# Optimization experiments

Hardware: AMD Instinct MI355X
Metric: run time of the kernel (lower is better)

The kernel has to match this reference:

```python
import jax, jax.numpy as jnp
import numpy as np
from jax import lax

S_DET, S_ANG = 725, 360   # detector bins, projection angles
OUT = 512                 # reconstructed image side
NNZ = 8388608             # nonzeros in sparse backprojection matrix AT
BATCH = 4
BN_EPS = 1e-3             # keras BatchNormalization default epsilon


def _ramp_filter():
    # w_bfunction(pi, linspace(-362, 362, 725))
    s = np.linspace(-np.floor(S_DET / 2), S_DET - np.floor(S_DET / 2) - 1, S_DET)
    v = np.pi * s
    u = np.empty_like(v)
    z = v == 0
    u[z] = 0.5
    nz = ~z
    u[nz] = (np.cos(v[nz]) - 1.0) / v[nz] ** 2 + np.sin(v[nz]) / v[nz]
    return (u * np.pi ** 2 / (4.0 * np.pi ** 2)).astype(np.float32)


def setup_inputs() -> dict:
    key = jax.random.key(0)
    ks = jax.random.split(key, 24)
    p = 0.05
    inp = {
        'inputs': jax.random.normal(ks[0], (BATCH, S_DET, S_ANG, 1), jnp.float32),
        'w_sin1': jax.random.normal(ks[1], (5, 5, 1, 64), jnp.float32) * p,
        'b_sin1': jnp.zeros((64,), jnp.float32),
        'w_sin_mid': jax.random.normal(ks[2], (4, 5, 5, 64, 64), jnp.float32) * p,
        'sin_gamma': jnp.ones((4, 64), jnp.float32),
        'sin_beta': jnp.zeros((4, 64), jnp.float32),
        'sin_mean': jax.random.normal(ks[3], (4, 64), jnp.float32) * 0.1,
        'sin_var': jax.random.uniform(ks[4], (4, 64), jnp.float32, 0.5, 1.5),
        'w_sin6': jax.random.normal(ks[5], (5, 5, 64, 1), jnp.float32) * p,
        'b_sin6': jnp.zeros((1,), jnp.float32),
        'w_ct1': jax.random.normal(ks[6], (5, 5, 1, 64), jnp.float32) * p,
        'b_ct1': jnp.zeros((64,), jnp.float32),
        'w_ct_mid': jax.random.normal(ks[7], (5, 5, 5, 64, 64), jnp.float32) * p,
        'ct_gamma': jnp.ones((5, 64), jnp.float32),
        'ct_beta': jnp.zeros((5, 64), jnp.float32),
        'ct_mean': jax.random.normal(ks[8], (5, 64), jnp.float32) * 0.1,
        'ct_var': jax.random.uniform(ks[9], (5, 64), jnp.float32, 0.5, 1.5),
        'w_ct6': jax.random.normal(ks[10], (5, 5, 64, 1), jnp.float32) * p,
        'b_ct6': jnp.zeros((1,), jnp.float32),
        'w_b': jnp.asarray(_ramp_filter()),
        'at_vals': jax.random.uniform(ks[11], (NNZ,), jnp.float32) * 1e-3,
        'at_rows': jnp.sort(jax.random.randint(ks[12], (NNZ,), 0, OUT * OUT, jnp.int32)),
        'at_cols': jax.random.randint(ks[13], (NNZ,), 0, S_DET * S_ANG, jnp.int32),
    }
    return inp


def _conv2d(x, w, b=None):
    y = lax.conv_general_dilated(x, w, (1, 1), 'SAME',
                                 dimension_numbers=('NHWC', 'HWIO', 'NHWC'))
    return y if b is None else y + b


def _bn(x, g, b, m, v):
    return (x - m) * (g * lax.rsqrt(v + BN_EPS)) + b


def _decode(sin_fan, w_b, at_vals, at_rows, at_cols):
    B = sin_fan.shape[0]
    sf = jnp.transpose(sin_fan, (0, 2, 1, 3))          # [B, 360, 725, 1]
    x = sf.reshape(-1, S_DET, 1)                       # [B*360, 725, 1]
    k = w_b.reshape(S_DET, 1, 1)
    f = lax.conv_general_dilated(x, k, (1,), 'SAME',
                                 dimension_numbers=('NWC', 'WIO', 'NWC'))
    f2 = f.reshape(B, -1).T                            # [261000, B]
    # sparse AT @ f2 via gather + segment_sum
    contrib = at_vals[:, None] * f2[at_cols]           # [nnz, B]
    rf = jax.ops.segment_sum(contrib, at_rows, num_segments=OUT * OUT)
    return 4.0 * rf.T.reshape(B, OUT, OUT, 1)


def reference(inputs, w_sin1, b_sin1, w_sin_mid, sin_gamma, sin_beta, sin_mean,
              sin_var, w_sin6, b_sin6, w_ct1, b_ct1, w_ct_mid, ct_gamma,
              ct_beta, ct_mean, ct_var, w_ct6, b_ct6, w_b, at_vals,
              at_rows, at_cols):
    # --- sinogram domain residual CNN ---
    de = jax.nn.relu(_conv2d(inputs, w_sin1, b_sin1))
    pp = de
    for i in range(4):  # M1 residual blocks
        de = jax.nn.relu(_bn(_conv2d(de, w_sin_mid[i]), sin_gamma[i],
                             sin_beta[i], sin_mean[i], sin_var[i]))
        pp = de + pp
    de_sin = _conv2d(pp / 4.0, w_sin6, b_sin6) + inputs
    # --- filtered backprojection ---
    fbp = _decode(de_sin, w_b, at_vals, at_rows, at_cols)
    # --- image domain residual CNN ---
    out = jax.nn.relu(_conv2d(fbp, w_ct1, b_ct1))
    qq = out
    for i in range(5):  # M2 residual blocks
        out = jax.nn.relu(_bn(_conv2d(out, w_ct_mid[i]), ct_gamma[i],
                              ct_beta[i], ct_mean[i], ct_var[i]))
        qq = qq + out
    outputs = _conv2d(qq / 5.0, w_ct6, b_ct6) + fbp
    return (de_sin, outputs, fbp)
```

## Files before the change

### kernel.cpp

```cpp
#include <hip/hip_runtime.h>
#include <stdint.h>

#define S_DET 725
#define S_ANG 360
#define OUTD  512
#define NB    4

typedef float    float4v __attribute__((ext_vector_type(4)));
typedef int      int4v   __attribute__((ext_vector_type(4)));
typedef _Float16 half8   __attribute__((ext_vector_type(8)));
typedef _Float16 half4   __attribute__((ext_vector_type(4)));
typedef _Float16 half2v  __attribute__((ext_vector_type(2)));

#define GAS __attribute__((address_space(1)))
#define LAS __attribute__((address_space(3)))

__device__ __forceinline__ void async16(const void* src, void* lds) {
  __builtin_amdgcn_global_load_lds((const GAS void*)(uintptr_t)src,
                                   (LAS void*)(uint32_t)(uintptr_t)lds, 16, 0, 0);
}

__global__ __launch_bounds__(256)
void prep_weights(const float* __restrict__ wsin, const float* __restrict__ sg,
                  const float* __restrict__ sb,  const float* __restrict__ sm,
                  const float* __restrict__ sv,
                  const float* __restrict__ wct, const float* __restrict__ cg,
                  const float* __restrict__ cbt, const float* __restrict__ cm,
                  const float* __restrict__ cv,
                  const float* __restrict__ wsin6, const float* __restrict__ wct6,
                  _Float16* __restrict__ wout, float* __restrict__ bout,
                  _Float16* __restrict__ w6out)
{
  int id = blockIdx.x * 256 + threadIdx.x;
  if (id < 9 * 102400) {
    int l   = id / 102400;
    int rem = id - l * 102400;
    int t = rem >> 12;
    int kn = rem & 4095;
    int k = kn >> 6, n = kn & 63;
    const float *w, *g, *b, *m, *v;
    if (l < 4) { w = wsin + l*102400; g = sg + l*64; b = sb + l*64; m = sm + l*64; v = sv + l*64; }
    else { int li = l - 4; w = wct + li*102400; g = cg + li*64; b = cbt + li*64; m = cm + li*64; v = cv + li*64; }
    float s = g[n] * rsqrtf(v[n] + 1e-3f);
    float val = w[rem] * s;
    int slot = (k >> 3) ^ (n & 7);
    wout[(size_t)l*102400 + t*4096 + n*64 + slot*8 + (k & 7)] = (_Float16)val;
    if (rem < 64)
      bout[l*64 + rem] = b[rem] - m[rem] * s;
  } else {
    int r = id - 9 * 102400;
    if (r < 3200)
      w6out[r] = (_Float16)(r < 1600 ? wsin6[r] : wct6[r - 1600]);
  }
}

template <int IMG>
__global__ __launch_bounds__(256)
void conv1_kernel(const float* __restrict__ src, _Float16* __restrict__ dst,
                  const float* __restrict__ w1, const float* __restrict__ b1,
                  int H, int W, int b0)
{
  __shared__ __align__(16) float in_s[400];
  __shared__ __align__(16) float w_s[1600];
  __shared__ float b_s[64];
  const int tid = threadIdx.x;
  const int bz = blockIdx.z, gb = b0 + bz;
  const int y0 = blockIdx.y * 16, x0 = blockIdx.x * 16;
  for (int i = tid; i < 1600; i += 256) w_s[i] = w1[i];
  if (tid < 64) b_s[tid] = b1[tid];
  for (int i = tid; i < 400; i += 256) {
    int iy = i / 20, ix = i - iy * 20;
    int y = y0 - 2 + iy, x = x0 - 2 + ix;
    float v = 0.f;
    if (y >= 0 && y < H && x >= 0 && x < W) {
      if (IMG) v = 4.f * src[(size_t)(y * W + x) * 4 + gb];
      else     v = src[((size_t)gb * H + y) * W + x];
    }
    in_s[i] = v;
  }
  __syncthreads();
  const int ty = tid >> 4, tx = tid & 15;
  float acc[64];
#pragma unroll
  for (int c = 0; c < 64; ++c) acc[c] = 0.f;
  int dy = 0, dx = 0;
  for (int t = 0; t < 25; ++t) {
    float v = in_s[(ty + dy) * 20 + tx + dx];
    const float4v* wp = (const float4v*)(w_s + t * 64);
#pragma unroll
    for (int c = 0; c < 16; ++c) {
      float4v w4 = wp[c];
      acc[4*c+0] += v * w4[0]; acc[4*c+1] += v * w4[1];
      acc[4*c+2] += v * w4[2]; acc[4*c+3] += v * w4[3];
    }
    if (++dx == 5) { dx = 0; ++dy; }
  }
  const int y = y0 + ty, x = x0 + tx;
  if (y < H && x < W) {
    uint32_t* dp = (uint32_t*)(dst + ((size_t)(bz * H + y) * W + x) * 64);
#pragma unroll
    for (int c = 0; c < 32; ++c) {
      float v0 = acc[2*c]   + b_s[2*c];   v0 = v0 > 0.f ? v0 : 0.f;
      float v1 = acc[2*c+1] + b_s[2*c+1]; v1 = v1 > 0.f ? v1 : 0.f;
      half2v h = { (_Float16)v0, (_Float16)v1 };
      dp[c] = __builtin_bit_cast(uint32_t, h);
    }
  }
}

__global__ __launch_bounds__(256, 2)
void mid_conv(const _Float16* __restrict__ src, _Float16* __restrict__ dst,
              float* __restrict__ accum,
              const _Float16* __restrict__ wt, const _Float16* __restrict__ w6g,
              const float* __restrict__ bias, const char* __restrict__ zbuf,
              int H, int W, int b0)
{
  __shared__ __align__(16) char smem[51200 + 2 * 8192 + 3200 + 16];
  char* const atile = smem;
  char* const wbuf  = smem + 51200;
  _Float16* const w6l = (_Float16*)(smem + 51200 + 16384);
  char* const zl = smem + 51200 + 16384 + 3200;
  const int tid = threadIdx.x;
  const int wv = tid >> 6, ln = tid & 63;
  const int bz = blockIdx.z, gb = b0 + bz;
  const int y0 = blockIdx.y * 16, x0 = blockIdx.x * 16;

  if (tid < 200) ((half8*)w6l)[tid] = ((const half8*)w6g)[tid];
  if (tid < 4) ((int*)zl)[tid] = 0;

  for (int inst = wv; inst < 50; inst += 4) {
    const int slot = inst * 64 + ln;
    const int p = slot >> 3, gp = slot & 7;
    const int g = gp ^ (p & 7);
    const int iy = p / 20, ix = p - iy * 20;
    const int y = y0 - 2 + iy, x = x0 - 2 + ix;
    const char* sp = (y >= 0 && y < H && x >= 0 && x < W)
        ? (const char*)(src + ((size_t)(bz * H + y) * W + x) * 64) + g * 16
        : zbuf + g * 16;
    async16(sp, atile + inst * 1024);
  }
#pragma unroll
  for (int j = 0; j < 2; ++j) {
    const int inst = wv * 2 + j;
    async16((const char*)wt + inst * 1024 + ln * 16, wbuf + inst * 1024);
  }
  __syncthreads();

  float4v acc[4][4];
  float4v acc6[4];
#pragma unroll
  for (int pi = 0; pi < 4; ++pi) {
    acc6[pi] = (float4v){0.f, 0.f, 0.f, 0.f};
#pragma unroll
    for (int ci = 0; ci < 4; ++ci) acc[pi][ci] = (float4v){0.f, 0.f, 0.f, 0.f};
  }

  int dy = 0, dx = 0;
  for (int t = 0; t < 25; ++t) {
    if (t < 24) {
      char* wdst = wbuf + ((t + 1) & 1) * 8192;
#pragma unroll
      for (int j = 0; j < 2; ++j) {
        const int inst = wv * 2 + j;
        async16((const char*)wt + (t + 1) * 8192 + inst * 1024 + ln * 16,
                wdst + inst * 1024);
      }
    }
    const char* wb = wbuf + (t & 1) * 8192;
#pragma unroll
    for (int kc = 0; kc < 2; ++kc) {
      const int g0 = kc * 4 + (ln >> 4);
      half8 wf[4], af[4], wf6;
#pragma unroll
      for (int ci = 0; ci < 4; ++ci) {
        const int ch = ci * 16 + (ln & 15);
        wf[ci] = *(const half8*)(wb + ch * 128 + ((g0 ^ (ch & 7)) << 4));
      }
      wf6 = *(const half8*)((ln & 15) == 0
                ? (const char*)(w6l + t * 64 + kc * 32 + ((ln >> 4) << 3))
                : zl);
#pragma unroll
      for (int pi = 0; pi < 4; ++pi) {
        const int p = (wv * 4 + pi + dy) * 20 + (ln & 15) + dx;
        af[pi] = *(const half8*)(atile + p * 128 + ((g0 ^ (p & 7)) << 4));
      }
#pragma unroll
      for (int pi = 0; pi < 4; ++pi) {
#pragma unroll
        for (int ci = 0; ci < 4; ++ci)
          acc[pi][ci] = __builtin_amdgcn_mfma_f32_16x16x32_f16(
              wf[ci], af[pi], acc[pi][ci], 0, 0, 0);
        acc6[pi] = __builtin_amdgcn_mfma_f32_16x16x32_f16(
            wf6, af[pi], acc6[pi], 0, 0, 0);
      }
    }
    if (++dx == 5) { dx = 0; ++dy; }
    __syncthreads();
  }

  const int tx = ln & 15;
  const int x = x0 + tx;
#pragma unroll
  for (int pi = 0; pi < 4; ++pi) {
    const int y = y0 + wv * 4 + pi;
    if (y < H && x < W) {
      _Float16* dp = dst + ((size_t)(bz * H + y) * W + x) * 64;
#pragma unroll
      for (int ci = 0; ci < 4; ++ci) {
        const int cbase = ci * 16 + (ln >> 4) * 4;
        const float4v bv = *(const float4v*)(bias + cbase);
        half4 h;
#pragma unroll
        for (int r = 0; r < 4; ++r) {
          float v = acc[pi][ci][r] + bv[r];
          v = v > 0.f ? v : 0.f;
          h[r] = (_Float16)v;
        }
        *(half4*)(dp + cbase) = h;
      }
    }
  }
  if (ln < 16) {
#pragma unroll
    for (int pi = 0; pi < 4; ++pi) {
      const int y = y0 + wv * 4 + pi, x2 = x0 + ln;
      if (y < H && x2 < W)
        accum[((size_t)gb * H + y) * W + x2] += acc6[pi][0];
    }
  }
}

__global__ __launch_bounds__(256, 2)
void fc_accum(const _Float16* __restrict__ src, float* __restrict__ accum,
              const float* __restrict__ w6, const char* __restrict__ zbuf,
              int H, int W, int b0)
{
  __shared__ __align__(16) char smem[51200 + 3200];
  char* const atile = smem;
  _Float16* const wl = (_Float16*)(smem + 51200);
  const int tid = threadIdx.x;
  const int wv = tid >> 6, ln = tid & 63;
  const int bz = blockIdx.z, gb = b0 + bz;
  const int y0 = blockIdx.y * 16, x0 = blockIdx.x * 16;
  for (int i = tid; i < 1600; i += 256) wl[i] = (_Float16)w6[i];
  for (int inst = wv; inst < 50; inst += 4) {
    const int slot = inst * 64 + ln;
    const int p = slot >> 3, gp = slot & 7;
    const int g = gp ^ (p & 7);
    const int iy = p / 20, ix = p - iy * 20;
    const int y = y0 - 2 + iy, x = x0 - 2 + ix;
    const char* sp = (y >= 0 && y < H && x >= 0 && x < W)
        ? (const char*)(src + ((size_t)(bz * H + y) * W + x) * 64) + g * 16
        : zbuf + g * 16;
    async16(sp, atile + inst * 1024);
  }
  __syncthreads();
  const int ty = tid >> 4, tx = tid & 15;
  float sum = 0.f;
  int dy = 0, dxx = 0;
  for (int t = 0; t < 25; ++t) {
    const int p = (ty + dy) * 20 + tx + dxx;
    const char* pb = atile + p * 128;
    const int pk = p & 7;
    const half2v* wp = (const half2v*)(wl + t * 64);
#pragma unroll
    for (int g = 0; g < 8; ++g) {
      half8 h = *(const half8*)(pb + ((g ^ pk) << 4));
#pragma unroll
      for (int q = 0; q < 4; ++q) {
        half2v a = { h[2*q], h[2*q+1] };
        sum = __builtin_amdgcn_fdot2(a, wp[g * 4 + q], sum, false);
      }
    }
    if (++dxx == 5) { dxx = 0; ++dy; }
  }
  const int y = y0 + ty, x = x0 + tx;
  if (y < H && x < W) accum[((size_t)gb * H + y) * W + x] += sum;
}

__global__ __launch_bounds__(256)
void write_desin(const float* __restrict__ accf, const float* __restrict__ inputs,
                 const float* __restrict__ b6, float* __restrict__ out)
{
  int id = blockIdx.x * 256 + threadIdx.x;
  if (id < NB * S_DET * S_ANG) out[id] = accf[id] * 0.25f + b6[0] + inputs[id];
}

__global__ __launch_bounds__(128)
void ramp_filter(const float* __restrict__ desin, const float* __restrict__ wb,
                 _Float16* __restrict__ f2h)
{
  __shared__ float col[1472];
  __shared__ float wl[725];
  const int blk = blockIdx.x;
  const int b = blk / 360, a = blk - b * 360;
  const int tid = threadIdx.x;
  for (int i = tid; i < 1472; i += 128) col[i] = 0.f;
  for (int i = tid; i < 725; i += 128) wl[i] = wb[i];
  __syncthreads();
  for (int i = tid; i < 725; i += 128) col[368 + i] = desin[(b * 725 + i) * 360 + a];
  __syncthreads();
  const int s0 = tid * 6;
  if (s0 < 725) {
    float o0 = 0, o1 = 0, o2 = 0, o3 = 0, o4 = 0, o5 = 0;
    const float* cb = col + 6 + s0;
    float r0 = cb[0], r1 = cb[1], r2 = cb[2], r3 = cb[3], r4 = cb[4], r5 = cb[5];
    for (int t = 0; t < 725; ++t) {
      float w = wl[t];
      o0 += r0 * w; o1 += r1 * w; o2 += r2 * w;
      o3 += r3 * w; o4 += r4 * w; o5 += r5 * w;
      r0 = r1; r1 = r2; r2 = r3; r3 = r4; r4 = r5; r5 = cb[t + 6];
    }
    float o[6] = { o0, o1, o2, o3, o4, o5 };
#pragma unroll
    for (int j = 0; j < 6; ++j)
      if (s0 + j < 725) f2h[((size_t)a * 725 + s0 + j) * 4 + b] = (_Float16)o[j];
  }
}

__global__ __launch_bounds__(256)
void backproj(const float* __restrict__ vals, const int* __restrict__ rows,
              const int* __restrict__ cols, const _Float16* __restrict__ f2h,
              float* __restrict__ rf)
{
  const int tid = blockIdx.x * 256 + threadIdx.x;
  const int i0 = tid * 16;
  const int4v* rp = (const int4v*)(rows + i0);
  const int4v* cp = (const int4v*)(cols + i0);
  const float4v* vp = (const float4v*)(vals + i0);
  float a0 = 0, a1 = 0, a2 = 0, a3 = 0;
  int4v r0v = __builtin_nontemporal_load(rp);
  int cur = r0v[0];
#pragma unroll
  for (int q = 0; q < 4; ++q) {
    int4v r4 = (q == 0) ? r0v : __builtin_nontemporal_load(rp + q);
    int4v c4 = __builtin_nontemporal_load(cp + q);
    float4v v4 = __builtin_nontemporal_load(vp + q);
#pragma unroll
    for (int u = 0; u < 4; ++u) {
      int r = r4[u]; int c = c4[u]; float v = v4[u];
      if (r != cur) {
        atomicAdd(rf + (size_t)cur * 4 + 0, a0);
        atomicAdd(rf + (size_t)cur * 4 + 1, a1);
        atomicAdd(rf + (size_t)cur * 4 + 2, a2);
        atomicAdd(rf + (size_t)cur * 4 + 3, a3);
        a0 = a1 = a2 = a3 = 0; cur = r;
      }
      const half4 f = *(const half4*)(f2h + (size_t)c * 4);
      a0 += v * (float)f[0]; a1 += v * (float)f[1];
      a2 += v * (float)f[2]; a3 += v * (float)f[3];
    }
  }
  atomicAdd(rf + (size_t)cur * 4 + 0, a0);
  atomicAdd(rf + (size_t)cur * 4 + 1, a1);
  atomicAdd(rf + (size_t)cur * 4 + 2, a2);
  atomicAdd(rf + (size_t)cur * 4 + 3, a3);
}

__global__ __launch_bounds__(256)
void write_fbp(const float* __restrict__ rf, float* __restrict__ out)
{
  int id = blockIdx.x * 256 + threadIdx.x;
  int b = id >> 18, p = id & 262143;
  out[id] = 4.f * rf[(size_t)p * 4 + b];
}

__global__ __launch_bounds__(256)
void write_outputs(const float* __restrict__ accf, const float* __restrict__ rf,
                   const float* __restrict__ b6, float* __restrict__ out)
{
  int id = blockIdx.x * 256 + threadIdx.x;
  int b = id >> 18, p = id & 262143;
  out[id] = accf[id] * 0.2f + b6[0] + 4.f * rf[(size_t)p * 4 + b];
}

extern "C" void kernel_launch(void* const* d_in, const int* in_sizes, int n_in,
                              void* d_out, int out_size, void* d_ws, size_t ws_size,
                              hipStream_t stream)
{
  (void)in_sizes; (void)n_in; (void)out_size;
  const float* inputs   = (const float*)d_in[0];
  const float* w_sin1   = (const float*)d_in[1];
  const float* b_sin1   = (const float*)d_in[2];
  const float* w_sin_mid= (const float*)d_in[3];
  const float* sin_gamma= (const float*)d_in[4];
  const float* sin_beta = (const float*)d_in[5];
  const float* sin_mean = (const float*)d_in[6];
  const float* sin_var  = (const float*)d_in[7];
  const float* w_sin6   = (const float*)d_in[8];
  const float* b_sin6   = (const float*)d_in[9];
  const float* w_ct1    = (const float*)d_in[10];
  const float* b_ct1    = (const float*)d_in[11];
  const float* w_ct_mid = (const float*)d_in[12];
  const float* ct_gamma = (const float*)d_in[13];
  const float* ct_beta  = (const float*)d_in[14];
  const float* ct_mean  = (const float*)d_in[15];
  const float* ct_var   = (const float*)d_in[16];
  const float* w_ct6    = (const float*)d_in[17];
  const float* b_ct6    = (const float*)d_in[18];
  const float* w_b      = (const float*)d_in[19];
  const float* at_vals  = (const float*)d_in[20];
  const int*   at_rows  = (const int*)d_in[21];
  const int*   at_cols  = (const int*)d_in[22];
  float* out = (float*)d_out;

  const size_t base = (size_t)11 << 20;
  const size_t act_per_batch = (size_t)2 * 262144 * 128;
  int nbat = 1;
  if (ws_size >= base + 4 * act_per_batch) nbat = 4;
  else if (ws_size >= base + 2 * act_per_batch) nbat = 2;
  const int npass = 4 / nbat;

  char* ws = (char*)d_ws;
  size_t off = 0;
  auto alloc = [&](size_t bytes) {
    char* p = ws + off;
    off = (off + bytes + 255) & ~(size_t)255;
    return p;
  };
  char*     zbuf    = alloc(256);
  _Float16* wmid    = (_Float16*)alloc((size_t)9 * 102400 * 2);
  float*    biasmid = (float*)alloc(9 * 64 * 4);
  _Float16* w6s     = (_Float16*)alloc(3200 * 2);
  float*    rf      = (float*)alloc((size_t)262144 * 16);
  char*     shreg   = alloc((size_t)262144 * 16);
  _Float16* act_a   = (_Float16*)alloc((size_t)nbat * 262144 * 128);
  _Float16* act_b   = (_Float16*)alloc((size_t)nbat * 262144 * 128);
  _Float16* f2h    = (_Float16*)shreg;
  float*    acc_fc = (float*)shreg;

  hipMemsetAsync(zbuf, 0, 256, stream);
  hipMemsetAsync(rf, 0, (size_t)262144 * 16, stream);
  hipMemsetAsync(acc_fc, 0, (size_t)262144 * 16, stream);

  prep_weights<<<3613, 256, 0, stream>>>(w_sin_mid, sin_gamma, sin_beta, sin_mean, sin_var,
                                         w_ct_mid, ct_gamma, ct_beta, ct_mean, ct_var,
                                         w_sin6, w_ct6, wmid, biasmid, w6s);

  for (int p = 0; p < npass; ++p) {
    const int b0 = p * nbat;
    conv1_kernel<0><<<dim3(23, 46, nbat), 256, 0, stream>>>(inputs, act_a, w_sin1, b_sin1,
                                                            725, 360, b0);
    _Float16* cur = act_a; _Float16* nxt = act_b;
    for (int i = 0; i < 4; ++i) {
      mid_conv<<<dim3(23, 46, nbat), 256, 0, stream>>>(cur, nxt, acc_fc,
                                                       wmid + (size_t)i * 102400, w6s,
                                                       biasmid + i * 64, zbuf, 725, 360, b0);
      _Float16* t = cur; cur = nxt; nxt = t;
    }
    fc_accum<<<dim3(23, 46, nbat), 256, 0, stream>>>(cur, acc_fc, w_sin6, zbuf, 725, 360, b0);
  }
  write_desin<<<4079, 256, 0, stream>>>(acc_fc, inputs, b_sin6, out);

  ramp_filter<<<1440, 128, 0, stream>>>(out, w_b, f2h);
  backproj<<<2048, 256, 0, stream>>>(at_vals, at_rows, at_cols, f2h, rf);
  write_fbp<<<4096, 256, 0, stream>>>(rf, out + 2092576);

  hipMemsetAsync(acc_fc, 0, (size_t)262144 * 16, stream);
  for (int p = 0; p < npass; ++p) {
    const int b0 = p * nbat;
    conv1_kernel<1><<<dim3(32, 32, nbat), 256, 0, stream>>>(rf, act_a, w_ct1, b_ct1,
                                                            512, 512, b0);
    _Float16* cur = act_a; _Float16* nxt = act_b;
    for (int i = 0; i < 5; ++i) {
      mid_conv<<<dim3(32, 32, nbat), 256, 0, stream>>>(cur, nxt, acc_fc,
                                                       wmid + (size_t)(4 + i) * 102400,
                                                       w6s + 1600,
                                                       biasmid + (4 + i) * 64, zbuf,
                                                       512, 512, b0);
      _Float16* t = cur; cur = nxt; nxt = t;
    }
    fc_accum<<<dim3(32, 32, nbat), 256, 0, stream>>>(cur, acc_fc, w_ct6, zbuf, 512, 512, b0);
  }
  write_outputs<<<4096, 256, 0, stream>>>(acc_fc, rf, b_ct6, out + 1044000);
}
```

Before: 2.752 ms.

## Read mid-conv weights directly from global memory and drop per-tap LDS staging

The weight prep kernel now writes weights in a fragment-major layout, so each lane's MFMA operand is one contiguous 16-byte global load. The mid conv kernel no longer double-buffers weights and the 1x1 head weights in LDS. That removes the per-tap __syncthreads and shrinks shared memory to the activation tile, and launch bounds are raised to 3 blocks per CU for more occupancy. The trade-off is that weight fetches now rely on L1/L2 cache hits and add global-load latency to the inner loop. The extra occupancy may also cost registers.

```diff
diff --git a/kernel.cpp b/kernel.cpp
--- a/kernel.cpp
+++ b/kernel.cpp
@@ -43,8 +43,9 @@
     else { int li = l - 4; w = wct + li*102400; g = cg + li*64; b = cbt + li*64; m = cm + li*64; v = cv + li*64; }
     float s = g[n] * rsqrtf(v[n] + 1e-3f);
     float val = w[rem] * s;
-    int slot = (k >> 3) ^ (n & 7);
-    wout[(size_t)l*102400 + t*4096 + n*64 + slot*8 + (k & 7)] = (_Float16)val;
+    int dst = t*4096 + (k >> 5)*2048 + (n >> 4)*512 + ((k >> 3) & 3)*128
+            + (n & 15)*8 + (k & 7);
+    wout[(size_t)l*102400 + dst] = (_Float16)val;
     if (rem < 64)
       bout[l*64 + rem] = b[rem] - m[rem] * s;
   } else {
@@ -108,25 +109,18 @@
   }
 }
 
-__global__ __launch_bounds__(256, 2)
+__global__ __launch_bounds__(256, 3)
 void mid_conv(const _Float16* __restrict__ src, _Float16* __restrict__ dst,
               float* __restrict__ accum,
               const _Float16* __restrict__ wt, const _Float16* __restrict__ w6g,
               const float* __restrict__ bias, const char* __restrict__ zbuf,
               int H, int W, int b0)
 {
-  __shared__ __align__(16) char smem[51200 + 2 * 8192 + 3200 + 16];
-  char* const atile = smem;
-  char* const wbuf  = smem + 51200;
-  _Float16* const w6l = (_Float16*)(smem + 51200 + 16384);
-  char* const zl = smem + 51200 + 16384 + 3200;
+  __shared__ __align__(16) char atile[51200];
   const int tid = threadIdx.x;
   const int wv = tid >> 6, ln = tid & 63;
   const int bz = blockIdx.z, gb = b0 + bz;
   const int y0 = blockIdx.y * 16, x0 = blockIdx.x * 16;
-
-  if (tid < 200) ((half8*)w6l)[tid] = ((const half8*)w6g)[tid];
-  if (tid < 4) ((int*)zl)[tid] = 0;
 
   for (int inst = wv; inst < 50; inst += 4) {
     const int slot = inst * 64 + ln;
@@ -139,11 +133,6 @@
         : zbuf + g * 16;
     async16(sp, atile + inst * 1024);
   }
-#pragma unroll
-  for (int j = 0; j < 2; ++j) {
-    const int inst = wv * 2 + j;
-    async16((const char*)wt + inst * 1024 + ln * 16, wbuf + inst * 1024);
-  }
   __syncthreads();
 
   float4v acc[4][4];
@@ -155,30 +144,21 @@
     for (int ci = 0; ci < 4; ++ci) acc[pi][ci] = (float4v){0.f, 0.f, 0.f, 0.f};
   }
 
+  const half8* const wbase = (const half8*)wt + ln;
+  const half8* const zl = (const half8*)zbuf;
+
   int dy = 0, dx = 0;
   for (int t = 0; t < 25; ++t) {
-    if (t < 24) {
-      char* wdst = wbuf + ((t + 1) & 1) * 8192;
-#pragma unroll
-      for (int j = 0; j < 2; ++j) {
-        const int inst = wv * 2 + j;
-        async16((const char*)wt + (t + 1) * 8192 + inst * 1024 + ln * 16,
-                wdst + inst * 1024);
-      }
-    }
-    const char* wb = wbuf + (t & 1) * 8192;
 #pragma unroll
     for (int kc = 0; kc < 2; ++kc) {
       const int g0 = kc * 4 + (ln >> 4);
       half8 wf[4], af[4], wf6;
-#pragma unroll
-      for (int ci = 0; ci < 4; ++ci) {
-        const int ch = ci * 16 + (ln & 15);
-        wf[ci] = *(const half8*)(wb + ch * 128 + ((g0 ^ (ch & 7)) << 4));
-      }
-      wf6 = *(const half8*)((ln & 15) == 0
-                ? (const char*)(w6l + t * 64 + kc * 32 + ((ln >> 4) << 3))
-                : zl);
+      const half8* wp = wbase + t * 512 + kc * 256;
+#pragma unroll
+      for (int ci = 0; ci < 4; ++ci) wf[ci] = wp[ci * 64];
+      wf6 = ((ln & 15) == 0)
+          ? *(const half8*)(w6g + t * 64 + kc * 32 + ((ln >> 4) << 3))
+          : *zl;
 #pragma unroll
       for (int pi = 0; pi < 4; ++pi) {
         const int p = (wv * 4 + pi + dy) * 20 + (ln & 15) + dx;
@@ -195,7 +175,6 @@
       }
     }
     if (++dx == 5) { dx = 0; ++dy; }
-    __syncthreads();
   }
 
   const int tx = ln & 15;
```

Measured after the change: 2.821 ms. 1.03x slower.
